# Kernel tuning notes

Measured on AMD Instinct MI355X. Metric: run time of the kernel, lower is better.

Reference implementation:

```python
import jax, jax.numpy as jnp
import numpy as np

D_MODEL = 2048
N_HEAD = 16
B, T = 2, 2048
D_HEAD = D_MODEL // N_HEAD          # 128
D_Q = D_MODEL // 3                  # 682
D_KV = D_MODEL // 2                 # 1024
D_QK_N = D_HEAD // 2                # 64
D_QK_R = D_HEAD // 2                # 64
LN_EPS = 1e-5


def setup_inputs() -> dict:
    key = jax.random.key(0)
    ks = jax.random.split(key, 8)
    s = 0.02
    return {
        'x': jax.random.normal(ks[0], (B, T, D_MODEL), dtype=jnp.float32),
        'Wdq_w': jax.random.normal(ks[1], (D_Q, D_MODEL), dtype=jnp.float32) * s,
        'Wdq_b': jnp.zeros((D_Q,), jnp.float32),
        'qn_g': jnp.ones((D_Q,), jnp.float32),
        'qn_b': jnp.zeros((D_Q,), jnp.float32),
        'Wuq_w': jax.random.normal(ks[2], (D_MODEL, D_Q), dtype=jnp.float32) * s,
        'Wuq_b': jnp.zeros((D_MODEL,), jnp.float32),
        'Wdkv_w': jax.random.normal(ks[3], (D_KV + D_QK_R, D_MODEL), dtype=jnp.float32) * s,
        'Wdkv_b': jnp.zeros((D_KV + D_QK_R,), jnp.float32),
        'kvn_g': jnp.ones((D_KV,), jnp.float32),
        'kvn_b': jnp.zeros((D_KV,), jnp.float32),
        'Wukv_w': jax.random.normal(ks[4], (D_MODEL + N_HEAD * D_QK_N, D_KV), dtype=jnp.float32) * s,
        'Wukv_b': jnp.zeros((D_MODEL + N_HEAD * D_QK_N,), jnp.float32),
        'Wo_w': jax.random.normal(ks[5], (D_MODEL, D_MODEL), dtype=jnp.float32) * s,
        'Wo_b': jnp.zeros((D_MODEL,), jnp.float32),
    }


def _linear(x, w, b):
    return jnp.einsum('...i,oi->...o', x, w) + b


def _layernorm(x, g, b):
    mu = jnp.mean(x, axis=-1, keepdims=True)
    var = jnp.mean(jnp.square(x - mu), axis=-1, keepdims=True)
    return (x - mu) * jax.lax.rsqrt(var + LN_EPS) * g + b


def _rotary(x):
    # Faithful to source: positions are taken from axis 1 of x (B, A, T, d)
    A, d = x.shape[1], x.shape[-1]
    inv_freq = (1.0 / 10000.0) ** (jnp.arange(0, d, 2, dtype=jnp.float32) / d)
    freqs = jnp.arange(A, dtype=jnp.float32)[:, None] * inv_freq[None, :]
    cos = jnp.cos(freqs)[None, :, None, :]
    sin = jnp.sin(freqs)[None, :, None, :]
    x1, x2 = jnp.split(x, 2, axis=-1)
    return jnp.concatenate([x1 * cos + x2 * sin, -x1 * sin + x2 * cos], axis=-1)


def reference(x, Wdq_w, Wdq_b, qn_g, qn_b, Wuq_w, Wuq_b,
              Wdkv_w, Wdkv_b, kvn_g, kvn_b, Wukv_w, Wukv_b, Wo_w, Wo_b):
    Bx, Tx, C = x.shape
    # Q path: down-proj -> norm -> up-proj
    c_q = _layernorm(_linear(x, Wdq_w, Wdq_b), qn_g, qn_b)
    q = _linear(c_q, Wuq_w, Wuq_b).reshape(Bx, Tx, N_HEAD, D_HEAD).transpose(0, 2, 1, 3)
    q_n, q_r = q[..., :D_QK_N], q[..., D_QK_N:]
    q_r = _rotary(q_r)
    # KV path
    c_kv = _linear(x, Wdkv_w, Wdkv_b)
    kv_n, k_r = c_kv[..., :D_KV], c_kv[..., D_KV:]
    kv_n = _layernorm(kv_n, kvn_g, kvn_b)
    kv = _linear(kv_n, Wukv_w, Wukv_b).reshape(Bx, Tx, N_HEAD, D_HEAD + D_QK_N).transpose(0, 2, 1, 3)
    k_n, v = kv[..., :D_QK_N], kv[..., D_QK_N:]
    k_r = k_r.reshape(Bx, Tx, 1, D_QK_R).transpose(0, 2, 1, 3)  # (B,1,T,dr)
    k_r = _rotary(k_r)  # identity here (single position), kept for fidelity
    k_r = jnp.broadcast_to(k_r, (Bx, N_HEAD, Tx, D_QK_R))
    q_full = jnp.concatenate([q_n, q_r], axis=-1)   # (B,H,T,d_head)
    k_full = jnp.concatenate([k_n, k_r], axis=-1)   # (B,H,T,d_head)
    # causal SDPA (scale = 1/sqrt(q dim))
    scale = 1.0 / np.sqrt(D_HEAD)
    scores = jnp.einsum('bhqd,bhkd->bhqk', q_full, k_full) * scale
    causal = jnp.tril(jnp.ones((Tx, Tx), dtype=bool))
    scores = jnp.where(causal[None, None], scores, jnp.finfo(scores.dtype).min)
    p = jax.nn.softmax(scores, axis=-1)
    y = jnp.einsum('bhqk,bhkd->bhqd', p, v)
    y = y.transpose(0, 2, 1, 3).reshape(Bx, Tx, C)
    return _linear(y, Wo_w, Wo_b)
```

## Files before the change

### kernel.cpp

```cpp
#include <hip/hip_runtime.h>
#include <math.h>

#define TOK 4096
#define DM 2048
#define DQ 682
#define DQP 704
#define DKV 1024
#define DUKV 3072
#define NH 16
#define T_SEQ 2048
#define NQKV 1792

typedef __attribute__((ext_vector_type(8))) short short8;
typedef __attribute__((ext_vector_type(4))) float floatx4;
typedef __attribute__((ext_vector_type(2))) unsigned int uint2v;

__device__ __forceinline__ unsigned short f2bf(float f) {
  union { float f; unsigned int u; } v; v.f = f;
  unsigned int u = v.u;
  u += 0x7fffu + ((u >> 16) & 1u);
  return (unsigned short)(u >> 16);
}
__device__ __forceinline__ unsigned short f2bf_fast(float f) {
  union { float f; unsigned int u; } v; v.f = f;
  return (unsigned short)((v.u + 0x8000u) >> 16);
}

typedef __attribute__((address_space(1))) const unsigned int as1_u32;
typedef __attribute__((address_space(3))) unsigned int as3_u32;
__device__ __forceinline__ void async16(const void* g, void* l) {
  __builtin_amdgcn_global_load_lds((as1_u32*)g, (as3_u32*)l, 16, 0, 0);
}

__global__ __launch_bounds__(256) void gemm_dqkv_sk(
    const unsigned short* __restrict__ A,
    const unsigned short* __restrict__ B,
    float* __restrict__ P0, float* __restrict__ P1)
{
  __shared__ __align__(16) unsigned short sm[16384];
  const int kz = blockIdx.z;
  const unsigned short* Ab = A + kz * 1024;
  const unsigned short* Bb = B + kz * 1024;
  float* C = kz ? P1 : P0;
  const int K = 1024;

  const int tid = threadIdx.x;
  const int w = tid >> 6, lane = tid & 63, q = lane >> 4, r = lane & 15;
  const int bm = blockIdx.y * 128, bn = blockIdx.x * 128;

  floatx4 acc[4][4];
#pragma unroll
  for (int i = 0; i < 4; i++)
#pragma unroll
    for (int j = 0; j < 4; j++) acc[i][j] = (floatx4){0.f, 0.f, 0.f, 0.f};

  const int srow = tid >> 2, scol = (tid & 3) * 8;
  const unsigned short* Ag0 = Ab + (size_t)(bm + srow) * 2048 + scol;
  const unsigned short* Ag1 = Ab + (size_t)(bm + 64 + srow) * 2048 + scol;
  const unsigned short* Bg0 = Bb + (size_t)(bn + srow) * 2048 + scol;
  const unsigned short* Bg1 = Bb + (size_t)(bn + 64 + srow) * 2048 + scol;
  const int mrow0 = (w >> 1) * 64, ncol0 = (w & 1) * 64;

  async16(Ag0, &sm[w * 512]);
  async16(Ag1, &sm[2048 + w * 512]);
  async16(Bg0, &sm[8192 + w * 512]);
  async16(Bg1, &sm[8192 + 2048 + w * 512]);

  for (int k0 = 0; k0 < K; k0 += 32) {
    const int cur = (k0 >> 5) & 1;
    __syncthreads();
    if (k0 + 32 < K) {
      const int nxt = cur ^ 1;
      async16(Ag0 + k0 + 32, &sm[nxt * 4096 + w * 512]);
      async16(Ag1 + k0 + 32, &sm[nxt * 4096 + 2048 + w * 512]);
      async16(Bg0 + k0 + 32, &sm[8192 + nxt * 4096 + w * 512]);
      async16(Bg1 + k0 + 32, &sm[8192 + nxt * 4096 + 2048 + w * 512]);
    }
    const unsigned short* As = &sm[cur * 4096];
    const unsigned short* Bs = &sm[8192 + cur * 4096];
    short8 a[4], b[4];
#pragma unroll
    for (int i = 0; i < 4; i++)
      a[i] = *(const short8*)&As[(mrow0 + i * 16 + r) * 32 + q * 8];
#pragma unroll
    for (int j = 0; j < 4; j++)
      b[j] = *(const short8*)&Bs[(ncol0 + j * 16 + r) * 32 + q * 8];
#pragma unroll
    for (int i = 0; i < 4; i++)
#pragma unroll
      for (int j = 0; j < 4; j++)
        acc[i][j] = __builtin_amdgcn_mfma_f32_16x16x32_bf16(a[i], b[j], acc[i][j], 0, 0, 0);
  }

#pragma unroll
  for (int j = 0; j < 4; j++) {
    int gc = bn + ncol0 + j * 16 + r;
#pragma unroll
    for (int i = 0; i < 4; i++) {
#pragma unroll
      for (int v = 0; v < 4; v++) {
        int gr = bm + mrow0 + i * 16 + q * 4 + v;
        C[(size_t)gr * NQKV + gc] = acc[i][j][v];
      }
    }
  }
}

__global__ __launch_bounds__(256) void gemm_wo64(
    const unsigned short* __restrict__ A,
    const unsigned short* __restrict__ B,
    const float* __restrict__ bias, float* __restrict__ C)
{
  __shared__ __align__(16) unsigned short sm[32768];
  const int tid = threadIdx.x;
  const int w = tid >> 6, lane = tid & 63, q = lane >> 4, r = lane & 15;
  const int bm = blockIdx.y * 128, bn = blockIdx.x * 128;

  floatx4 acc[4][4];
#pragma unroll
  for (int i = 0; i < 4; i++)
#pragma unroll
    for (int j = 0; j < 4; j++) acc[i][j] = (floatx4){0.f, 0.f, 0.f, 0.f};

  const int srow = tid >> 2, scol = (tid & 3) * 8;
  const unsigned short* Ag0 = A + (size_t)(bm + srow) * 2048 + scol;
  const unsigned short* Ag1 = A + (size_t)(bm + 64 + srow) * 2048 + scol;
  const unsigned short* Bg0 = B + (size_t)(bn + srow) * 2048 + scol;
  const unsigned short* Bg1 = B + (size_t)(bn + 64 + srow) * 2048 + scol;
  const int mrow0 = (w >> 1) * 64, ncol0 = (w & 1) * 64;

#pragma unroll
  for (int c2 = 0; c2 < 2; c2++) {
    async16(Ag0 + c2 * 32, &sm[c2 * 4096 + w * 512]);
    async16(Ag1 + c2 * 32, &sm[c2 * 4096 + 2048 + w * 512]);
    async16(Bg0 + c2 * 32, &sm[16384 + c2 * 4096 + w * 512]);
    async16(Bg1 + c2 * 32, &sm[16384 + c2 * 4096 + 2048 + w * 512]);
  }

  for (int k0 = 0; k0 < 2048; k0 += 64) {
    const int cur = (k0 >> 6) & 1;
    __syncthreads();
    if (k0 + 64 < 2048) {
      const int nxt = cur ^ 1;
#pragma unroll
      for (int c2 = 0; c2 < 2; c2++) {
        async16(Ag0 + k0 + 64 + c2 * 32, &sm[nxt * 8192 + c2 * 4096 + w * 512]);
        async16(Ag1 + k0 + 64 + c2 * 32, &sm[nxt * 8192 + c2 * 4096 + 2048 + w * 512]);
        async16(Bg0 + k0 + 64 + c2 * 32, &sm[16384 + nxt * 8192 + c2 * 4096 + w * 512]);
        async16(Bg1 + k0 + 64 + c2 * 32, &sm[16384 + nxt * 8192 + c2 * 4096 + 2048 + w * 512]);
      }
    }
#pragma unroll
    for (int c2 = 0; c2 < 2; c2++) {
      const unsigned short* As = &sm[cur * 8192 + c2 * 4096];
      const unsigned short* Bs = &sm[16384 + cur * 8192 + c2 * 4096];
      short8 a[4], b[4];
#pragma unroll
      for (int i = 0; i < 4; i++)
        a[i] = *(const short8*)&As[(mrow0 + i * 16 + r) * 32 + q * 8];
#pragma unroll
      for (int j = 0; j < 4; j++)
        b[j] = *(const short8*)&Bs[(ncol0 + j * 16 + r) * 32 + q * 8];
#pragma unroll
      for (int i = 0; i < 4; i++)
#pragma unroll
        for (int j = 0; j < 4; j++)
          acc[i][j] = __builtin_amdgcn_mfma_f32_16x16x32_bf16(a[i], b[j], acc[i][j], 0, 0, 0);
    }
  }

#pragma unroll
  for (int j = 0; j < 4; j++) {
    int gc = bn + ncol0 + j * 16 + r;
    float bv = bias[gc];
#pragma unroll
    for (int i = 0; i < 4; i++) {
#pragma unroll
      for (int v = 0; v < 4; v++) {
        int gr = bm + mrow0 + i * 16 + q * 4 + v;
        C[(size_t)gr * 2048 + gc] = acc[i][j][v] + bv;
      }
    }
  }
}

__global__ __launch_bounds__(256) void gemm_up_fused(
    const unsigned short* __restrict__ Aq, const unsigned short* __restrict__ Bq,
    const float* __restrict__ biasq, unsigned short* __restrict__ Qall,
    const unsigned short* __restrict__ Akv, const unsigned short* __restrict__ Bkv,
    const float* __restrict__ biaskv,
    unsigned short* __restrict__ Kn, unsigned short* __restrict__ Vb)
{
  __shared__ __align__(16) unsigned short sm[16384];
  const int tid = threadIdx.x;
  const int w = tid >> 6, lane = tid & 63, q = lane >> 4, r = lane & 15;
  const int bx = blockIdx.x;
  const bool isQ = bx < 16;
  const int bn = isQ ? bx * 128 : (bx - 16) * 128;
  const int bm = blockIdx.y * 128;
  const int K = isQ ? DQP : DKV;
  const unsigned short* A = isQ ? Aq : Akv;
  const unsigned short* B = isQ ? Bq : Bkv;

  floatx4 acc[4][4];
#pragma unroll
  for (int i = 0; i < 4; i++)
#pragma unroll
    for (int j = 0; j < 4; j++) acc[i][j] = (floatx4){0.f, 0.f, 0.f, 0.f};

  const int srow = tid >> 2, scol = (tid & 3) * 8;
  const unsigned short* Ag0 = A + (size_t)(bm + srow) * K + scol;
  const unsigned short* Ag1 = A + (size_t)(bm + 64 + srow) * K + scol;
  const unsigned short* Bg0 = B + (size_t)(bn + srow) * K + scol;
  const unsigned short* Bg1 = B + (size_t)(bn + 64 + srow) * K + scol;
  const int mrow0 = (w >> 1) * 64, ncol0 = (w & 1) * 64;

  async16(Ag0, &sm[w * 512]);
  async16(Ag1, &sm[2048 + w * 512]);
  async16(Bg0, &sm[8192 + w * 512]);
  async16(Bg1, &sm[8192 + 2048 + w * 512]);

  for (int k0 = 0; k0 < K; k0 += 32) {
    const int cur = (k0 >> 5) & 1;
    __syncthreads();
    if (k0 + 32 < K) {
      const int nxt = cur ^ 1;
      async16(Ag0 + k0 + 32, &sm[nxt * 4096 + w * 512]);
      async16(Ag1 + k0 + 32, &sm[nxt * 4096 + 2048 + w * 512]);
      async16(Bg0 + k0 + 32, &sm[8192 + nxt * 4096 + w * 512]);
      async16(Bg1 + k0 + 32, &sm[8192 + nxt * 4096 + 2048 + w * 512]);
    }
    const unsigned short* As = &sm[cur * 4096];
    const unsigned short* Bs = &sm[8192 + cur * 4096];
    short8 a[4], b[4];
#pragma unroll
    for (int i = 0; i < 4; i++)
      a[i] = *(const short8*)&As[(mrow0 + i * 16 + r) * 32 + q * 8];
#pragma unroll
    for (int j = 0; j < 4; j++)
      b[j] = *(const short8*)&Bs[(ncol0 + j * 16 + r) * 32 + q * 8];
#pragma unroll
    for (int i = 0; i < 4; i++)
#pragma unroll
      for (int j = 0; j < 4; j++)
        acc[i][j] = __builtin_amdgcn_mfma_f32_16x16x32_bf16(a[i], b[j], acc[i][j], 0, 0, 0);
  }

  if (!isQ) {
#pragma unroll
    for (int j = 0; j < 4; j++) {
      int gc = bn + ncol0 + j * 16 + r;
      float bv = biaskv[gc];
      int hh = gc / 192;
      int rel = gc - hh * 192;
#pragma unroll
      for (int i = 0; i < 4; i++) {
#pragma unroll
        for (int v = 0; v < 4; v++) {
          int gr = bm + mrow0 + i * 16 + q * 4 + v;
          int bb = gr >> 11, tt = gr & 2047;
          int bhh = bb * NH + hh;
          int kt = tt >> 6;
          unsigned short val = f2bf(acc[i][j][v] + bv);
          if (rel < 64) {
            Kn[((size_t)(bhh * 32 + kt)) * 4096 + (rel >> 5) * 2048 +
               (tt & 63) * 32 + ((rel & 31) ^ (((tt >> 1) & 3) << 3))] = val;
          } else {
            int d = rel - 64;
            Vb[((size_t)(bhh * 32 + kt)) * 8192 + ((tt >> 5) & 1) * 4096 +
               d * 32 + ((tt & 31) ^ (((d >> 1) & 3) << 3))] = val;
          }
        }
      }
    }
    return;
  }

  const int h = bx;
  const float QS = (float)(0.08838834764831845 * 1.4426950408889634);
  if ((w & 1) == 0) {
#pragma unroll
    for (int j = 0; j < 4; j++) {
      int d = j * 16 + r;
      float bv = biasq[h * 128 + d];
#pragma unroll
      for (int i = 0; i < 4; i++) {
#pragma unroll
        for (int v = 0; v < 4; v++) {
          int gr = bm + mrow0 + i * 16 + q * 4 + v;
          int bb = gr >> 11, t = gr & 2047;
          Qall[(((size_t)(bb * NH + h)) * T_SEQ + t) * 128 + d] =
              f2bf((acc[i][j][v] + bv) * QS);
        }
      }
    }
  } else {
    float cs[2], sn[2], bv1[2], bv2[2];
#pragma unroll
    for (int jp = 0; jp < 2; jp++) {
      int jj = jp * 16 + r;
      float ang = (float)h * exp2f(-(float)jj * (13.287712379549449f / 32.0f));
      cs[jp] = cosf(ang); sn[jp] = sinf(ang);
      bv1[jp] = biasq[h * 128 + 64 + jj];
      bv2[jp] = biasq[h * 128 + 96 + jj];
    }
#pragma unroll
    for (int i = 0; i < 4; i++) {
#pragma unroll
      for (int v = 0; v < 4; v++) {
        int gr = bm + mrow0 + i * 16 + q * 4 + v;
        int bb = gr >> 11, t = gr & 2047;
        unsigned short* Qr = Qall + (((size_t)(bb * NH + h)) * T_SEQ + t) * 128;
#pragma unroll
        for (int jp = 0; jp < 2; jp++) {
          int jj = jp * 16 + r;
          float x1 = acc[i][jp][v] + bv1[jp];
          float x2 = acc[i][jp + 2][v] + bv2[jp];
          Qr[64 + jj] = f2bf((x1 * cs[jp] + x2 * sn[jp]) * QS);
          Qr[96 + jj] = f2bf((x2 * cs[jp] - x1 * sn[jp]) * QS);
        }
      }
    }
  }
}

__device__ __forceinline__ void cvt_region(
    const float* __restrict__ in, unsigned short* __restrict__ out,
    int irows, int icols, int ocols, long idx)
{
  int rr = (int)(idx / ocols);
  int cc = (int)(idx - (long)rr * ocols);
  out[idx] = (rr < irows && cc < icols) ? f2bf(in[(size_t)rr * icols + cc]) : 0;
}

__global__ __launch_bounds__(256) void prep_all(
    const float* __restrict__ x,
    const float* __restrict__ Wdq_w, const float* __restrict__ Wdkv_w,
    const float* __restrict__ Wuq_w, const float* __restrict__ Wukv_w,
    const float* __restrict__ Wo_w,
    const float* __restrict__ Wdq_b, const float* __restrict__ Wdkv_b,
    unsigned short* __restrict__ x_bf,
    unsigned short* __restrict__ Wqkv_bf, unsigned short* __restrict__ Wuq_bf,
    unsigned short* __restrict__ Wukv_bf, unsigned short* __restrict__ Wo_bf,
    float* __restrict__ bias_qkv)
{
  const long bx = blockIdx.x;
  if (bx < 32768) {
    long idx = bx * 256 + threadIdx.x;
    x_bf[idx] = f2bf(x[idx]);
  } else if (bx < 38400) {
    cvt_region(Wdq_w, Wqkv_bf, 682, 2048, 2048, (bx - 32768) * 256 + threadIdx.x);
  } else if (bx < 47104) {
    cvt_region(Wdkv_w, Wqkv_bf + 704L * 2048, 1088, 2048, 2048,
               (bx - 38400) * 256 + threadIdx.x);
  } else if (bx < 52736) {
    cvt_region(Wuq_w, Wuq_bf, 2048, 682, 704, (bx - 47104) * 256 + threadIdx.x);
  } else if (bx < 65024) {
    cvt_region(Wukv_w, Wukv_bf, 3072, 1024, 1024, (bx - 52736) * 256 + threadIdx.x);
  } else if (bx < 81408) {
    cvt_region(Wo_w, Wo_bf, 2048, 2048, 2048, (bx - 65024) * 256 + threadIdx.x);
  } else {
    int i = (int)(bx - 81408) * 256 + threadIdx.x;
    if (i < NQKV)
      bias_qkv[i] = (i < DQ) ? Wdq_b[i] : ((i < DQP) ? 0.f : Wdkv_b[i - DQP]);
  }
}

__global__ __launch_bounds__(256) void ln_dual_r(
    const float* __restrict__ p0, const float* __restrict__ p1,
    const float* __restrict__ bqkv,
    unsigned short* __restrict__ outq, unsigned short* __restrict__ outkv,
    unsigned short* __restrict__ Kr,
    const float* __restrict__ qg, const float* __restrict__ qb2,
    const float* __restrict__ kg, const float* __restrict__ kb2)
{
  __shared__ float sbuf[8];
  const int blk = blockIdx.x;
  if (blk >= 8192) {
    const int base = (blk - 8192) * 512;
#pragma unroll
    for (int s = 0; s < 2; s++) {
      int idx = base + s * 256 + threadIdx.x;
      int row = idx >> 6, dr = idx & 63;
      size_t off = (size_t)row * NQKV + 1728 + dr;
      float v = p0[off] + p1[off] + bqkv[1728 + dr];
      Kr[((size_t)((row >> 11) * 32 + ((row & 2047) >> 6))) * 4096 +
         (dr >> 5) * 2048 + (row & 63) * 32 +
         ((dr & 31) ^ (((row >> 1) & 3) << 3))] = f2bf(v);
    }
    return;
  }
  const bool isQ = blk < 4096;
  const int r2 = isQ ? blk : blk - 4096;
  const int off = isQ ? 0 : DQP;
  const float* x0 = p0 + (size_t)r2 * NQKV + off;
  const float* x1 = p1 + (size_t)r2 * NQKV + off;
  const float* bb = bqkv + off;
  const int D = isQ ? DQ : DKV;
  const int ocols = isQ ? DQP : DKV;
  const float* g = isQ ? qg : kg;
  const float* bta = isQ ? qb2 : kb2;
  unsigned short* orow = (isQ ? outq : outkv) + (size_t)r2 * ocols;

  float s = 0.f, s2 = 0.f;
  float vv[4];
#pragma unroll
  for (int ii = 0; ii < 4; ii++) {
    int i = threadIdx.x + ii * 256;
    if (i < D) {
      float v = x0[i] + x1[i] + bb[i];
      vv[ii] = v;
      s += v; s2 += v * v;
    }
  }
#pragma unroll
  for (int o = 32; o > 0; o >>= 1) {
    s += __shfl_down(s, o, 64);
    s2 += __shfl_down(s2, o, 64);
  }
  int wid = threadIdx.x >> 6;
  __syncthreads();
  if ((threadIdx.x & 63) == 0) { sbuf[wid] = s; sbuf[4 + wid] = s2; }
  __syncthreads();
  float su = sbuf[0] + sbuf[1] + sbuf[2] + sbuf[3];
  float sq = sbuf[4] + sbuf[5] + sbuf[6] + sbuf[7];
  float mu = su / (float)D;
  float var = sq / (float)D - mu * mu;
  float rstd = rsqrtf(var + 1e-5f);
#pragma unroll
  for (int ii = 0; ii < 4; ii++) {
    int i = threadIdx.x + ii * 256;
    if (i < ocols)
      orow[i] = (i < D) ? f2bf((vv[ii] - mu) * rstd * g[i] + bta[i]) : 0;
  }
}

__global__ __launch_bounds__(256, 2) void attn_mfma8(
    const unsigned short* __restrict__ Qall,
    const unsigned short* __restrict__ Kn,
    const unsigned short* __restrict__ Kr,
    const unsigned short* __restrict__ Vb,
    unsigned short* __restrict__ y)
{
  __shared__ __align__(16) unsigned short sm[37376];
  const int id = (int)blockIdx.x;
  const int bhid = id & 31;
  const int idx = (id >> 5) & 7;
  const int qt = (id >= 256) ? (15 - idx) : idx;
  const int h = bhid & 15, b = bhid >> 4;
  const int tid = threadIdx.x;
  const int w = tid >> 6, lane = tid & 63, q = lane >> 4, r = lane & 15;
  const int bh = bhid;
  const int sq8 = (q ^ ((r >> 1) & 3)) * 8;

  const char* KnG = (const char*)(Kn + (size_t)bh * 32 * 4096);
  const char* KrG = (const char*)(Kr + (size_t)b * 32 * 4096);
  const char* VG  = (const char*)(Vb + (size_t)bh * 32 * 8192);
  char* smB = (char*)sm;
  unsigned short* Psw = sm + 32768 + w * 1152;
  const int ktmax = 2 * qt + 1;

#define PREFETCH_KV(kt_, buf_)                                                 \
  {                                                                            \
    const char* kn_ = KnG + (size_t)(kt_) * 8192;                              \
    const char* kr_ = KrG + (size_t)(kt_) * 8192;                              \
    const char* vg_ = VG + (size_t)(kt_) * 16384;                              \
    char* kd_ = smB + (buf_) * 16384;                                          \
    char* vd_ = smB + 32768 + (buf_) * 16384;                                  \
    _Pragma("unroll")                                                          \
    for (int i_ = 0; i_ < 2; i_++) {                                           \
      async16(kn_ + i_ * 4096 + w * 1024 + lane * 16,                          \
              kd_ + i_ * 4096 + w * 1024);                                     \
      async16(kr_ + i_ * 4096 + w * 1024 + lane * 16,                          \
              kd_ + 8192 + i_ * 4096 + w * 1024);                              \
    }                                                                          \
    _Pragma("unroll")                                                          \
    for (int i_ = 0; i_ < 4; i_++)                                             \
      async16(vg_ + i_ * 4096 + w * 1024 + lane * 16,                          \
              vd_ + i_ * 4096 + w * 1024);                                     \
  }

  PREFETCH_KV(0, 0);

  short8 qb[2][4];
#pragma unroll
  for (int g = 0; g < 2; g++) {
    const unsigned short* Qrow =
        Qall + ((size_t)bh * T_SEQ + (size_t)qt * 128 + w * 32 + g * 16 + r) * 128 + q * 8;
#pragma unroll
    for (int c = 0; c < 4; c++) qb[g][c] = *(const short8*)(Qrow + c * 32);
  }

  floatx4 oacc[2][8];
#pragma unroll
  for (int g = 0; g < 2; g++)
#pragma unroll
    for (int jd = 0; jd < 8; jd++) oacc[g][jd] = (floatx4){0.f, 0.f, 0.f, 0.f};
  float m_i[2] = {-3.0e38f, -3.0e38f}, l_i[2] = {0.f, 0.f};

  for (int kt = 0; kt <= ktmax; kt++) {
    const int cur = kt & 1;
    __syncthreads();
    if (kt < ktmax) PREFETCH_KV(kt + 1, cur ^ 1);

    const bool activeW = (kt * 64 <= qt * 128 + w * 32 + 31);
    if (activeW) {
      const unsigned short* KsC = sm + cur * 8192;
      const unsigned short* VsC = sm + 16384 + cur * 8192;

      floatx4 sacc[2][4];
#pragma unroll
      for (int g = 0; g < 2; g++)
#pragma unroll
        for (int j = 0; j < 4; j++) sacc[g][j] = (floatx4){0.f, 0.f, 0.f, 0.f};
      __builtin_amdgcn_s_setprio(1);
#pragma unroll
      for (int c = 0; c < 4; c++) {
        short8 ak[4];
#pragma unroll
        for (int j = 0; j < 4; j++)
          ak[j] = *(const short8*)&KsC[c * 2048 + (j * 16 + r) * 32 + sq8];
#pragma unroll
        for (int g = 0; g < 2; g++)
#pragma unroll
          for (int j = 0; j < 4; j++)
            sacc[g][j] = __builtin_amdgcn_mfma_f32_16x16x32_bf16(ak[j], qb[g][c], sacc[g][j], 0, 0, 0);
      }
      __builtin_amdgcn_s_setprio(0);

      short8 pb[2][2];
#pragma unroll
      for (int g = 0; g < 2; g++) {
        float sv[16];
#pragma unroll
        for (int j = 0; j < 4; j++)
#pragma unroll
          for (int v = 0; v < 4; v++) sv[j * 4 + v] = sacc[g][j][v];
        const int rel = qt * 128 + w * 32 + g * 16 + r - kt * 64;
        if (rel < 63) {
#pragma unroll
          for (int j = 0; j < 4; j++)
#pragma unroll
            for (int v = 0; v < 4; v++)
              if (j * 16 + q * 4 + v > rel) sv[j * 4 + v] = -3.0e38f;
        }
        float tm[8];
#pragma unroll
        for (int t = 0; t < 8; t++) tm[t] = fmaxf(sv[t], sv[t + 8]);
#pragma unroll
        for (int t = 0; t < 4; t++) tm[t] = fmaxf(tm[t], tm[t + 4]);
        float rm = fmaxf(fmaxf(tm[0], tm[2]), fmaxf(tm[1], tm[3]));
        rm = fmaxf(rm, __shfl_xor(rm, 16, 64));
        rm = fmaxf(rm, __shfl_xor(rm, 32, 64));
        if (__any(rm > m_i[g] + 8.f)) {
          float mnew = fmaxf(m_i[g], rm);
          float alpha = exp2f(m_i[g] - mnew);
          m_i[g] = mnew;
          l_i[g] *= alpha;
#pragma unroll
          for (int jd = 0; jd < 8; jd++) {
            oacc[g][jd][0] *= alpha; oacc[g][jd][1] *= alpha;
            oacc[g][jd][2] *= alpha; oacc[g][jd][3] *= alpha;
          }
        }
        float p[16];
#pragma unroll
        for (int t = 0; t < 16; t++) p[t] = exp2f(sv[t] - m_i[g]);
        float ts[8];
#pragma unroll
        for (int t = 0; t < 8; t++) ts[t] = p[t] + p[t + 8];
#pragma unroll
        for (int t = 0; t < 4; t++) ts[t] = ts[t] + ts[t + 4];
        float rsum = (ts[0] + ts[2]) + (ts[1] + ts[3]);
        rsum += __shfl_xor(rsum, 16, 64);
        rsum += __shfl_xor(rsum, 32, 64);
        l_i[g] += rsum;
#pragma unroll
        for (int j = 0; j < 4; j++) {
          unsigned int lo = (unsigned int)f2bf_fast(p[j * 4 + 0]) |
                            ((unsigned int)f2bf_fast(p[j * 4 + 1]) << 16);
          unsigned int hi = (unsigned int)f2bf_fast(p[j * 4 + 2]) |
                            ((unsigned int)f2bf_fast(p[j * 4 + 3]) << 16);
          uint2v pk; pk[0] = lo; pk[1] = hi;
          *(uint2v*)&Psw[r * 72 + j * 16 + q * 4] = pk;
        }
        pb[g][0] = *(const short8*)&Psw[r * 72 + q * 8];
        pb[g][1] = *(const short8*)&Psw[r * 72 + 32 + q * 8];
      }

      __builtin_amdgcn_s_setprio(1);
#pragma unroll
      for (int c2 = 0; c2 < 2; c2++) {
#pragma unroll
        for (int jd = 0; jd < 8; jd++) {
          short8 bv = *(const short8*)&VsC[c2 * 4096 + (jd * 16 + r) * 32 + sq8];
          oacc[0][jd] = __builtin_amdgcn_mfma_f32_16x16x32_bf16(bv, pb[0][c2], oacc[0][jd], 0, 0, 0);
          oacc[1][jd] = __builtin_amdgcn_mfma_f32_16x16x32_bf16(bv, pb[1][c2], oacc[1][jd], 0, 0, 0);
        }
      }
      __builtin_amdgcn_s_setprio(0);
    }
  }

#pragma unroll
  for (int g = 0; g < 2; g++) {
    float inv = 1.0f / l_i[g];
    unsigned short* yr =
        y + ((size_t)(b * T_SEQ) + (size_t)qt * 128 + w * 32 + g * 16 + r) * DM + h * 128;
#pragma unroll
    for (int jd = 0; jd < 8; jd++) {
      unsigned short o0 = f2bf(oacc[g][jd][0] * inv);
      unsigned short o1 = f2bf(oacc[g][jd][1] * inv);
      unsigned short o2 = f2bf(oacc[g][jd][2] * inv);
      unsigned short o3 = f2bf(oacc[g][jd][3] * inv);
      unsigned int lo = (unsigned int)o0 | ((unsigned int)o1 << 16);
      unsigned int hi = (unsigned int)o2 | ((unsigned int)o3 << 16);
      unsigned int* dst = (unsigned int*)(yr + jd * 16 + q * 4);
      dst[0] = lo; dst[1] = hi;
    }
  }
#undef PREFETCH_KV
}

extern "C" void kernel_launch(void* const* d_in, const int* in_sizes, int n_in,
                              void* d_out, int out_size, void* d_ws, size_t ws_size,
                              hipStream_t stream) {
  const float* x      = (const float*)d_in[0];
  const float* Wdq_w  = (const float*)d_in[1];
  const float* Wdq_b  = (const float*)d_in[2];
  const float* qn_g   = (const float*)d_in[3];
  const float* qn_b   = (const float*)d_in[4];
  const float* Wuq_w  = (const float*)d_in[5];
  const float* Wuq_b  = (const float*)d_in[6];
  const float* Wdkv_w = (const float*)d_in[7];
  const float* Wdkv_b = (const float*)d_in[8];
  const float* kvn_g  = (const float*)d_in[9];
  const float* kvn_b  = (const float*)d_in[10];
  const float* Wukv_w = (const float*)d_in[11];
  const float* Wukv_b = (const float*)d_in[12];
  const float* Wo_w   = (const float*)d_in[13];
  const float* Wo_b   = (const float*)d_in[14];
  float* out = (float*)d_out;

  float* ws = (float*)d_ws;
  unsigned short* x_bf    = (unsigned short*)(ws);
  unsigned short* y_bf    = (unsigned short*)(ws);
  unsigned short* Wqkv_bf = (unsigned short*)(ws + 4194304);
  unsigned short* Wuq_bf  = (unsigned short*)(ws + 6029312);
  unsigned short* Wukv_bf = (unsigned short*)(ws + 6750208);
  float* bias_qkv = ws + 8323072;
  float* p0       = ws + 8324864;
  float* p1       = ws + 15664896;
  unsigned short* c_q_bf = (unsigned short*)(ws + 23004928);
  unsigned short* kvn_bf = (unsigned short*)(ws + 24446720);
  unsigned short* Q_all  = (unsigned short*)(ws + 26543872);
  unsigned short* Kn_blk = (unsigned short*)(ws + 30738176);
  unsigned short* Kr_blk = (unsigned short*)(ws + 32835328);
  unsigned short* V_blk  = (unsigned short*)(ws + 32966400);
  unsigned short* Wo_bf  = (unsigned short*)(ws + 37160704);

  dim3 blk(256);

  prep_all<<<81415, blk, 0, stream>>>(x, Wdq_w, Wdkv_w, Wuq_w, Wukv_w, Wo_w,
                                      Wdq_b, Wdkv_b,
                                      x_bf, Wqkv_bf, Wuq_bf, Wukv_bf, Wo_bf,
                                      bias_qkv);
  gemm_dqkv_sk<<<dim3(14, 32, 2), blk, 0, stream>>>(x_bf, Wqkv_bf, p0, p1);
  ln_dual_r<<<8704, blk, 0, stream>>>(p0, p1, bias_qkv, c_q_bf, kvn_bf, Kr_blk,
                                      qn_g, qn_b, kvn_g, kvn_b);
  gemm_up_fused<<<dim3(40, 32), blk, 0, stream>>>(c_q_bf, Wuq_bf, Wuq_b, Q_all,
                                                  kvn_bf, Wukv_bf, Wukv_b,
                                                  Kn_blk, V_blk);
  attn_mfma8<<<512, blk, 0, stream>>>(Q_all, Kn_blk, Kr_blk, V_blk, y_bf);
  gemm_wo64<<<dim3(16, 32), blk, 0, stream>>>(y_bf, Wo_bf, Wo_b, out);
}
```

Baseline: 406.1 us.

## Load K/V fragments directly from global memory instead of staging through LDS

The attention kernel drops the double-buffered async LDS staging of K and V tiles along with the per-tile block barriers. Each wave now reads its MFMA operand fragments straight from global memory into registers, and the producer kernels stop applying the XOR swizzle that only served LDS bank-conflict avoidance. The goal is to remove barrier stalls and LDS traffic, and to let inactive waves skip whole tiles. The cost is that the four waves of a block re-read the same K/V tiles from global/L2, with no software prefetch to hide that latency, and register pressure goes up.

```diff
diff --git a/kernel.cpp b/kernel.cpp
--- a/kernel.cpp
+++ b/kernel.cpp
@@ -264,11 +264,11 @@
           unsigned short val = f2bf(acc[i][j][v] + bv);
           if (rel < 64) {
             Kn[((size_t)(bhh * 32 + kt)) * 4096 + (rel >> 5) * 2048 +
-               (tt & 63) * 32 + ((rel & 31) ^ (((tt >> 1) & 3) << 3))] = val;
+               (tt & 63) * 32 + (rel & 31)] = val;
           } else {
             int d = rel - 64;
             Vb[((size_t)(bhh * 32 + kt)) * 8192 + ((tt >> 5) & 1) * 4096 +
-               d * 32 + ((tt & 31) ^ (((d >> 1) & 3) << 3))] = val;
+               d * 32 + (tt & 31)] = val;
           }
         }
       }
@@ -385,8 +385,7 @@
       size_t off = (size_t)row * NQKV + 1728 + dr;
       float v = p0[off] + p1[off] + bqkv[1728 + dr];
       Kr[((size_t)((row >> 11) * 32 + ((row & 2047) >> 6))) * 4096 +
-         (dr >> 5) * 2048 + (row & 63) * 32 +
-         ((dr & 31) ^ (((row >> 1) & 3) << 3))] = f2bf(v);
+         (dr >> 5) * 2048 + (row & 63) * 32 + (dr & 31)] = f2bf(v);
     }
     return;
   }
@@ -435,14 +434,14 @@
   }
 }
 
-__global__ __launch_bounds__(256, 2) void attn_mfma8(
+__global__ __launch_bounds__(256, 2) void attn_mfma9(
     const unsigned short* __restrict__ Qall,
     const unsigned short* __restrict__ Kn,
     const unsigned short* __restrict__ Kr,
     const unsigned short* __restrict__ Vb,
     unsigned short* __restrict__ y)
 {
-  __shared__ __align__(16) unsigned short sm[37376];
+  __shared__ __align__(16) unsigned short Pswb[4608];
   const int id = (int)blockIdx.x;
   const int bhid = id & 31;
   const int idx = (id >> 5) & 7;
@@ -451,36 +450,12 @@
   const int tid = threadIdx.x;
   const int w = tid >> 6, lane = tid & 63, q = lane >> 4, r = lane & 15;
   const int bh = bhid;
-  const int sq8 = (q ^ ((r >> 1) & 3)) * 8;
-
-  const char* KnG = (const char*)(Kn + (size_t)bh * 32 * 4096);
-  const char* KrG = (const char*)(Kr + (size_t)b * 32 * 4096);
-  const char* VG  = (const char*)(Vb + (size_t)bh * 32 * 8192);
-  char* smB = (char*)sm;
-  unsigned short* Psw = sm + 32768 + w * 1152;
+
+  const unsigned short* KnT0 = Kn + (size_t)bh * 131072;
+  const unsigned short* KrT0 = Kr + (size_t)b * 131072;
+  const unsigned short* VT0  = Vb + (size_t)bh * 262144;
+  unsigned short* Psw = Pswb + w * 1152;
   const int ktmax = 2 * qt + 1;
-
-#define PREFETCH_KV(kt_, buf_)                                                 \
-  {                                                                            \
-    const char* kn_ = KnG + (size_t)(kt_) * 8192;                              \
-    const char* kr_ = KrG + (size_t)(kt_) * 8192;                              \
-    const char* vg_ = VG + (size_t)(kt_) * 16384;                              \
-    char* kd_ = smB + (buf_) * 16384;                                          \
-    char* vd_ = smB + 32768 + (buf_) * 16384;                                  \
-    _Pragma("unroll")                                                          \
-    for (int i_ = 0; i_ < 2; i_++) {                                           \
-      async16(kn_ + i_ * 4096 + w * 1024 + lane * 16,                          \
-              kd_ + i_ * 4096 + w * 1024);                                     \
-      async16(kr_ + i_ * 4096 + w * 1024 + lane * 16,                          \
-              kd_ + 8192 + i_ * 4096 + w * 1024);                              \
-    }                                                                          \
-    _Pragma("unroll")                                                          \
-    for (int i_ = 0; i_ < 4; i_++)                                             \
-      async16(vg_ + i_ * 4096 + w * 1024 + lane * 16,                          \
-              vd_ + i_ * 4096 + w * 1024);                                     \
-  }
-
-  PREFETCH_KV(0, 0);
 
   short8 qb[2][4];
 #pragma unroll
@@ -499,107 +474,114 @@
   float m_i[2] = {-3.0e38f, -3.0e38f}, l_i[2] = {0.f, 0.f};
 
   for (int kt = 0; kt <= ktmax; kt++) {
-    const int cur = kt & 1;
-    __syncthreads();
-    if (kt < ktmax) PREFETCH_KV(kt + 1, cur ^ 1);
-
     const bool activeW = (kt * 64 <= qt * 128 + w * 32 + 31);
-    if (activeW) {
-      const unsigned short* KsC = sm + cur * 8192;
-      const unsigned short* VsC = sm + 16384 + cur * 8192;
-
-      floatx4 sacc[2][4];
-#pragma unroll
-      for (int g = 0; g < 2; g++)
-#pragma unroll
-        for (int j = 0; j < 4; j++) sacc[g][j] = (floatx4){0.f, 0.f, 0.f, 0.f};
+    if (!activeW) continue;
+    const unsigned short* KnT = KnT0 + kt * 4096;
+    const unsigned short* KrT = KrT0 + kt * 4096;
+    const unsigned short* VT  = VT0 + kt * 8192;
+
+    floatx4 sacc[2][4];
+#pragma unroll
+    for (int g = 0; g < 2; g++)
+#pragma unroll
+      for (int j = 0; j < 4; j++) sacc[g][j] = (floatx4){0.f, 0.f, 0.f, 0.f};
+    {
+      short8 ak[4][4];
+#pragma unroll
+      for (int c = 0; c < 4; c++) {
+        const unsigned short* Ksrc = (c < 2) ? (KnT + c * 2048) : (KrT + (c - 2) * 2048);
+#pragma unroll
+        for (int j = 0; j < 4; j++)
+          ak[c][j] = *(const short8*)&Ksrc[(j * 16 + r) * 32 + q * 8];
+      }
       __builtin_amdgcn_s_setprio(1);
 #pragma unroll
-      for (int c = 0; c < 4; c++) {
-        short8 ak[4];
+      for (int c = 0; c < 4; c++)
+#pragma unroll
+        for (int g = 0; g < 2; g++)
+#pragma unroll
+          for (int j = 0; j < 4; j++)
+            sacc[g][j] = __builtin_amdgcn_mfma_f32_16x16x32_bf16(ak[c][j], qb[g][c], sacc[g][j], 0, 0, 0);
+      __builtin_amdgcn_s_setprio(0);
+    }
+
+    short8 vb[2][8];
+#pragma unroll
+    for (int c2 = 0; c2 < 2; c2++)
+#pragma unroll
+      for (int jd = 0; jd < 8; jd++)
+        vb[c2][jd] = *(const short8*)&VT[c2 * 4096 + (jd * 16 + r) * 32 + q * 8];
+
+    short8 pb[2][2];
+#pragma unroll
+    for (int g = 0; g < 2; g++) {
+      float sv[16];
+#pragma unroll
+      for (int j = 0; j < 4; j++)
+#pragma unroll
+        for (int v = 0; v < 4; v++) sv[j * 4 + v] = sacc[g][j][v];
+      const int rel = qt * 128 + w * 32 + g * 16 + r - kt * 64;
+      if (rel < 63) {
 #pragma unroll
         for (int j = 0; j < 4; j++)
-          ak[j] = *(const short8*)&KsC[c * 2048 + (j * 16 + r) * 32 + sq8];
-#pragma unroll
-        for (int g = 0; g < 2; g++)
-#pragma unroll
-          for (int j = 0; j < 4; j++)
-            sacc[g][j] = __builtin_amdgcn_mfma_f32_16x16x32_bf16(ak[j], qb[g][c], sacc[g][j], 0, 0, 0);
-      }
-      __builtin_amdgcn_s_setprio(0);
-
-      short8 pb[2][2];
-#pragma unroll
-      for (int g = 0; g < 2; g++) {
-        float sv[16];
-#pragma unroll
-        for (int j = 0; j < 4; j++)
-#pragma unroll
-          for (int v = 0; v < 4; v++) sv[j * 4 + v] = sacc[g][j][v];
-        const int rel = qt * 128 + w * 32 + g * 16 + r - kt * 64;
-        if (rel < 63) {
-#pragma unroll
-          for (int j = 0; j < 4; j++)
-#pragma unroll
-            for (int v = 0; v < 4; v++)
-              if (j * 16 + q * 4 + v > rel) sv[j * 4 + v] = -3.0e38f;
+#pragma unroll
+          for (int v = 0; v < 4; v++)
+            if (j * 16 + q * 4 + v > rel) sv[j * 4 + v] = -3.0e38f;
+      }
+      float tm[8];
+#pragma unroll
+      for (int t = 0; t < 8; t++) tm[t] = fmaxf(sv[t], sv[t + 8]);
+#pragma unroll
+      for (int t = 0; t < 4; t++) tm[t] = fmaxf(tm[t], tm[t + 4]);
+      float rm = fmaxf(fmaxf(tm[0], tm[2]), fmaxf(tm[1], tm[3]));
+      rm = fmaxf(rm, __shfl_xor(rm, 16, 64));
+      rm = fmaxf(rm, __shfl_xor(rm, 32, 64));
+      if (__any(rm > m_i[g] + 8.f)) {
+        float mnew = fmaxf(m_i[g], rm);
+        float alpha = exp2f(m_i[g] - mnew);
+        m_i[g] = mnew;
+        l_i[g] *= alpha;
+#pragma unroll
+        for (int jd = 0; jd < 8; jd++) {
+          oacc[g][jd][0] *= alpha; oacc[g][jd][1] *= alpha;
+          oacc[g][jd][2] *= alpha; oacc[g][jd][3] *= alpha;
         }
-        float tm[8];
-#pragma unroll
-        for (int t = 0; t < 8; t++) tm[t] = fmaxf(sv[t], sv[t + 8]);
-#pragma unroll
-        for (int t = 0; t < 4; t++) tm[t] = fmaxf(tm[t], tm[t + 4]);
-        float rm = fmaxf(fmaxf(tm[0], tm[2]), fmaxf(tm[1], tm[3]));
-        rm = fmaxf(rm, __shfl_xor(rm, 16, 64));
-        rm = fmaxf(rm, __shfl_xor(rm, 32, 64));
-        if (__any(rm > m_i[g] + 8.f)) {
-          float mnew = fmaxf(m_i[g], rm);
-          float alpha = exp2f(m_i[g] - mnew);
-          m_i[g] = mnew;
-          l_i[g] *= alpha;
-#pragma unroll
-          for (int jd = 0; jd < 8; jd++) {
-            oacc[g][jd][0] *= alpha; oacc[g][jd][1] *= alpha;
-            oacc[g][jd][2] *= alpha; oacc[g][jd][3] *= alpha;
-          }
-        }
-        float p[16];
-#pragma unroll
-        for (int t = 0; t < 16; t++) p[t] = exp2f(sv[t] - m_i[g]);
-        float ts[8];
-#pragma unroll
-        for (int t = 0; t < 8; t++) ts[t] = p[t] + p[t + 8];
-#pragma unroll
-        for (int t = 0; t < 4; t++) ts[t] = ts[t] + ts[t + 4];
-        float rsum = (ts[0] + ts[2]) + (ts[1] + ts[3]);
-        rsum += __shfl_xor(rsum, 16, 64);
-        rsum += __shfl_xor(rsum, 32, 64);
-        l_i[g] += rsum;
-#pragma unroll
-        for (int j = 0; j < 4; j++) {
-          unsigned int lo = (unsigned int)f2bf_fast(p[j * 4 + 0]) |
-                            ((unsigned int)f2bf_fast(p[j * 4 + 1]) << 16);
-          unsigned int hi = (unsigned int)f2bf_fast(p[j * 4 + 2]) |
-                            ((unsigned int)f2bf_fast(p[j * 4 + 3]) << 16);
-          uint2v pk; pk[0] = lo; pk[1] = hi;
-          *(uint2v*)&Psw[r * 72 + j * 16 + q * 4] = pk;
-        }
-        pb[g][0] = *(const short8*)&Psw[r * 72 + q * 8];
-        pb[g][1] = *(const short8*)&Psw[r * 72 + 32 + q * 8];
-      }
-
-      __builtin_amdgcn_s_setprio(1);
-#pragma unroll
-      for (int c2 = 0; c2 < 2; c2++) {
-#pragma unroll
-        for (int jd = 0; jd < 8; jd++) {
-          short8 bv = *(const short8*)&VsC[c2 * 4096 + (jd * 16 + r) * 32 + sq8];
-          oacc[0][jd] = __builtin_amdgcn_mfma_f32_16x16x32_bf16(bv, pb[0][c2], oacc[0][jd], 0, 0, 0);
-          oacc[1][jd] = __builtin_amdgcn_mfma_f32_16x16x32_bf16(bv, pb[1][c2], oacc[1][jd], 0, 0, 0);
-        }
-      }
-      __builtin_amdgcn_s_setprio(0);
-    }
+      }
+      float p[16];
+#pragma unroll
+      for (int t = 0; t < 16; t++) p[t] = exp2f(sv[t] - m_i[g]);
+      float ts[8];
+#pragma unroll
+      for (int t = 0; t < 8; t++) ts[t] = p[t] + p[t + 8];
+#pragma unroll
+      for (int t = 0; t < 4; t++) ts[t] = ts[t] + ts[t + 4];
+      float rsum = (ts[0] + ts[2]) + (ts[1] + ts[3]);
+      rsum += __shfl_xor(rsum, 16, 64);
+      rsum += __shfl_xor(rsum, 32, 64);
+      l_i[g] += rsum;
+#pragma unroll
+      for (int j = 0; j < 4; j++) {
+        unsigned int lo = (unsigned int)f2bf_fast(p[j * 4 + 0]) |
+                          ((unsigned int)f2bf_fast(p[j * 4 + 1]) << 16);
+        unsigned int hi = (unsigned int)f2bf_fast(p[j * 4 + 2]) |
+                          ((unsigned int)f2bf_fast(p[j * 4 + 3]) << 16);
+        uint2v pk; pk[0] = lo; pk[1] = hi;
+        *(uint2v*)&Psw[r * 72 + j * 16 + q * 4] = pk;
+      }
+      pb[g][0] = *(const short8*)&Psw[r * 72 + q * 8];
+      pb[g][1] = *(const short8*)&Psw[r * 72 + 32 + q * 8];
+    }
+
+    __builtin_amdgcn_s_setprio(1);
+#pragma unroll
+    for (int c2 = 0; c2 < 2; c2++) {
+#pragma unroll
+      for (int jd = 0; jd < 8; jd++) {
+        oacc[0][jd] = __builtin_amdgcn_mfma_f32_16x16x32_bf16(vb[c2][jd], pb[0][c2], oacc[0][jd], 0, 0, 0);
+        oacc[1][jd] = __builtin_amdgcn_mfma_f32_16x16x32_bf16(vb[c2][jd], pb[1][c2], oacc[1][jd], 0, 0, 0);
+      }
+    }
+    __builtin_amdgcn_s_setprio(0);
   }
 
 #pragma unroll
@@ -619,7 +601,6 @@
       dst[0] = lo; dst[1] = hi;
     }
   }
-#undef PREFETCH_KV
 }
 
 extern "C" void kernel_launch(void* const* d_in, const int* in_sizes, int n_in,
@@ -671,6 +652,6 @@
   gemm_up_fused<<<dim3(40, 32), blk, 0, stream>>>(c_q_bf, Wuq_bf, Wuq_b, Q_all,
                                                   kvn_bf, Wukv_bf, Wukv_b,
                                                   Kn_blk, V_blk);
-  attn_mfma8<<<512, blk, 0, stream>>>(Q_all, Kn_blk, Kr_blk, V_blk, y_bf);
+  attn_mfma9<<<512, blk, 0, stream>>>(Q_all, Kn_blk, Kr_blk, V_blk, y_bf);
   gemm_wo64<<<dim3(16, 32), blk, 0, stream>>>(y_bf, Wo_bf, Wo_b, out);
 }
```

Result: slower. 416.5 us (+2.6%).
